# Kernel tuning notes

Hardware: AMD Instinct MI355X
Metric: run time of the kernel (lower is better)

## Reference

```python
import jax, jax.numpy as jnp
import numpy as np

NUM_HEADS = 12
HEAD_SIZE = 64  # hidden 768 / 12 heads


def setup_inputs() -> dict:
    key = jax.random.key(0)
    ks = jax.random.split(key, 5)
    B, M, P, H = 8, 4, 512, 768
    scale = 1.0 / np.sqrt(H)
    return {
        "hidden_states": jax.random.normal(ks[0], (B, M, P, H), dtype=jnp.float32),
        "Wq": jax.random.normal(ks[1], (H, H), dtype=jnp.float32) * scale,
        "bq": jnp.zeros((H,), dtype=jnp.float32),
        "Wk": jax.random.normal(ks[2], (H, H), dtype=jnp.float32) * scale,
        "bk": jnp.zeros((H,), dtype=jnp.float32),
        "Wv": jax.random.normal(ks[3], (H, H), dtype=jnp.float32) * scale,
        "bv": jnp.zeros((H,), dtype=jnp.float32),
        "Wo": jax.random.normal(ks[4], (H, H), dtype=jnp.float32) * scale,
        "bo": jnp.zeros((H,), dtype=jnp.float32),
    }


def reference(hidden_states, Wq, bq, Wk, bk, Wv, bv, Wo, bo):
    # hidden_states: [B, M, P, H] (batch, modalities, patches, hidden)
    B, M, P, H = hidden_states.shape
    nh, hs = NUM_HEADS, HEAD_SIZE

    def split_heads(x):  # [B,M,P,H] -> [B,M,nh,P,hs]
        return x.reshape(B, M, P, nh, hs).transpose(0, 1, 3, 2, 4)

    q = split_heads(hidden_states @ Wq + bq)
    k = split_heads(hidden_states @ Wk + bk)
    v = split_heads(hidden_states @ Wv + bv)

    # per-modality, per-head attention over patches
    scores = jnp.einsum('bmnqh,bmnkh->bmnqk', q, k) / np.sqrt(hs).astype(jnp.float32)
    probs = jax.nn.softmax(scores, axis=-1)  # [B,M,nh,P,P]
    ctx = jnp.einsum('bmnqk,bmnkh->bmnqh', probs, v)
    ctx = ctx.transpose(0, 1, 3, 2, 4).reshape(B, M, P, H)  # merge heads

    # output projection (dropout rate 0.0 -> identity)
    return ctx @ Wo + bo
```

## Files before the change

### kernel.cpp

```cpp
#include <hip/hip_runtime.h>
#include <cstdint>
#include <cstddef>

#define H_DIM 768
#define NHEADS 12
#define HSZ 64
#define PATCH 512
#define MTOT 16384
#define SZT ((long)MTOT * H_DIM)

using short8 = __attribute__((ext_vector_type(8))) short;
using f32x4  = __attribute__((ext_vector_type(4))) float;
using us4    = __attribute__((ext_vector_type(4))) unsigned short;

#define GLL16(gp, lp) __builtin_amdgcn_global_load_lds( \
    (const __attribute__((address_space(1))) void*)(gp), \
    (__attribute__((address_space(3))) void*)(lp), 16, 0, 0)

#define SB0() __builtin_amdgcn_sched_barrier(0)

__device__ __forceinline__ unsigned short bf16rne(float x) {
    unsigned v = __float_as_uint(x);
    v += 0x7fff + ((v >> 16) & 1);
    return (unsigned short)(v >> 16);
}

__global__ __launch_bounds__(256) void prep_all(
    const float* __restrict__ X, unsigned short* __restrict__ Xb,
    const float* __restrict__ Wq, const float* __restrict__ Wk,
    const float* __restrict__ Wv, const float* __restrict__ Wo,
    unsigned short* __restrict__ WqH, unsigned short* __restrict__ WkH,
    unsigned short* __restrict__ WvH, unsigned short* __restrict__ WoH)
{
    __shared__ float T[64][65];
    const int b = blockIdx.x;
    const int tid = threadIdx.x;

    if (b < 6144) {
        const long i = ((long)b * 256 + tid) * 8;
        float4 a = *(const float4*)&X[i];
        float4 c = *(const float4*)&X[i + 4];
        float xs[8] = {a.x, a.y, a.z, a.w, c.x, c.y, c.z, c.w};
        us4 h0, h1;
        #pragma unroll
        for (int j = 0; j < 4; ++j) { h0[j] = bf16rne(xs[j]); h1[j] = bf16rne(xs[j + 4]); }
        *(us4*)&Xb[i] = h0; *(us4*)&Xb[i + 4] = h1;
        return;
    }

    const int w     = b - 6144;
    const int which = w / 144;
    const int t     = w % 144;
    const int kt    = (t / 12) * 64, nt = (t % 12) * 64;
    const float* W  = (which == 0) ? Wq : (which == 1) ? Wk : (which == 2) ? Wv : Wo;
    unsigned short* Whi = (which == 0) ? WqH : (which == 1) ? WkH : (which == 2) ? WvH : WoH;

    const int r = tid >> 2, c16 = (tid & 3) * 16;
    #pragma unroll
    for (int j = 0; j < 4; ++j) {
        float4 v = *(const float4*)&W[(long)(kt + r) * H_DIM + nt + c16 + j * 4];
        T[r][c16 + j*4 + 0] = v.x; T[r][c16 + j*4 + 1] = v.y;
        T[r][c16 + j*4 + 2] = v.z; T[r][c16 + j*4 + 3] = v.w;
    }
    __syncthreads();
    unsigned short* ph = &Whi[(long)(nt + r) * H_DIM + kt + c16];
    #pragma unroll
    for (int j = 0; j < 16; ++j)
        ph[j] = bf16rne(T[c16 + j][r]);
}

__global__ __launch_bounds__(256, 2) void qkv_gemm(
    const unsigned short* __restrict__ Xb,
    const unsigned short* __restrict__ WqH, const unsigned short* __restrict__ WkH,
    const unsigned short* __restrict__ WvH,
    const float* __restrict__ bq, const float* __restrict__ bk, const float* __restrict__ bv,
    float qscale,
    unsigned short* __restrict__ Qt, unsigned short* __restrict__ Kp,
    unsigned short* __restrict__ Vp)
{
    __shared__ unsigned short As[16384];
    __shared__ unsigned short Bs[8192];

    const int s   = blockIdx.x;
    const int lid = (s & 7) * 144 + (s >> 3);
    const int bx  = lid % 18;
    const int by  = lid / 18;

    const int mat = bx / 6;
    const int n0  = (bx % 6) * 128;
    const int m0  = by * 256;
    const unsigned short* Bh = (mat == 0) ? WqH : (mat == 1) ? WkH : WvH;
    const float* bias        = (mat == 0) ? bq  : (mat == 1) ? bk  : bv;
    const float scale        = (mat == 0) ? qscale : 1.0f;

    const int tid  = threadIdx.x;
    const int lane = tid & 63;
    const int wv   = tid >> 6;
    const int wr   = wv >> 1, wc = wv & 1;
    const int q    = lane >> 4, l15 = lane & 15;

    const int srow   = tid >> 3;
    const int schunk = (tid & 7) ^ (srow & 7);

    char* ldsA = (char*)(&As[0]) + (wv << 10);
    char* ldsB = (char*)(&Bs[0]) + (wv << 10);

    f32x4 acc[8][4];
    #pragma unroll
    for (int i = 0; i < 8; ++i)
        #pragma unroll
        for (int j = 0; j < 4; ++j) acc[i][j] = 0;

    const int swz = (l15 & 7);

    for (int k0 = 0; k0 < H_DIM; k0 += 64) {
        #pragma unroll
        for (int i = 0; i < 8; ++i)
            GLL16(Xb + (long)(m0 + i * 32 + srow) * H_DIM + k0 + schunk * 8,
                  ldsA + i * 4096);
        #pragma unroll
        for (int i = 0; i < 4; ++i)
            GLL16(Bh + (long)(n0 + i * 32 + srow) * H_DIM + k0 + schunk * 8,
                  ldsB + i * 4096);
        __syncthreads();

        #pragma unroll
        for (int ks = 0; ks < 2; ++ks) {
            const int pc = ((ks * 4 + q) ^ swz) * 8;
            short8 ah[8], bh[4];
            #pragma unroll
            for (int t = 0; t < 8; ++t) {
                const int mr = wr * 128 + t * 16 + l15;
                ah[t] = *(const short8*)&As[mr * 64 + pc];
            }
            #pragma unroll
            for (int t = 0; t < 4; ++t) {
                const int nr = wc * 64 + t * 16 + l15;
                bh[t] = *(const short8*)&Bs[nr * 64 + pc];
            }
            #pragma unroll
            for (int mt = 0; mt < 8; ++mt)
                #pragma unroll
                for (int nt = 0; nt < 4; ++nt)
                    acc[mt][nt] = __builtin_amdgcn_mfma_f32_16x16x32_bf16(ah[mt], bh[nt], acc[mt][nt], 0, 0, 0);
        }
        __syncthreads();
    }

    #pragma unroll
    for (int nt = 0; nt < 4; ++nt) {
        const int col = n0 + wc * 64 + nt * 16 + l15;
        const float bcol = bias[col];
        const int h = col >> 6, d = col & 63;
        #pragma unroll
        for (int mt = 0; mt < 8; ++mt) {
            const int rowB = m0 + wr * 128 + mt * 16 + q * 4;
            #pragma unroll
            for (int r = 0; r < 4; ++r) {
                const int row = rowB + r;
                const float val = (acc[mt][nt][r] + bcol) * scale;
                const int bm = row >> 9, p = row & 511;
                const int bmh = bm * NHEADS + h;
                if (mat == 0) {
                    const long idx = ((long)bmh * 8 + (p >> 6)) * 4096 + (long)(p & 63) * 64 + d;
                    Qt[idx] = bf16rne(val);
                } else if (mat == 1) {
                    Kp[(long)bmh * 32768 + (long)p * 64 + d] = bf16rne(val);
                } else {
                    Vp[(long)bmh * 32768 + (long)d * 512 + p] = bf16rne(val);
                }
            }
        }
    }
}

__global__ __launch_bounds__(256, 3) void attn2(
    const unsigned short* __restrict__ Qt,
    const unsigned short* __restrict__ Kp, const unsigned short* __restrict__ Vp,
    unsigned short* __restrict__ Ctx)
{
    __shared__ unsigned short Ks[2][4096];
    __shared__ unsigned short Vs[2][4096];
    __shared__ unsigned short Ps[128 * 72];
    __shared__ float red[128][2];

    const int tid  = threadIdx.x;
    const int lane = tid & 63;
    const int wv   = tid >> 6;
    const int wr   = wv >> 1, wc = wv & 1;
    const int q    = lane >> 4, l15 = lane & 15;

    const int s   = blockIdx.x + 4 * blockIdx.y;
    const int lid = (s & 7) * 192 + (s >> 3);
    const int qt2 = lid & 3;
    const int bmh = lid >> 2;

    short8 qh[4][2];
    const long qtile = ((long)bmh * 8 + qt2 * 2 + wr) * 4096;
    #pragma unroll
    for (int mt = 0; mt < 4; ++mt)
        #pragma unroll
        for (int ks = 0; ks < 2; ++ks)
            qh[mt][ks] = *(const short8*)&Qt[qtile + (mt * 16 + l15) * 64 + ks * 32 + q * 8];

    f32x4 ctx[4][2];
    float l_cur[4][4];
    #pragma unroll
    for (int mt = 0; mt < 4; ++mt) {
        ctx[mt][0] = 0; ctx[mt][1] = 0;
        #pragma unroll
        for (int r = 0; r < 4; ++r) l_cur[mt][r] = 0.0f;
    }

    const long khead = (long)bmh * 32768;
    const int srow   = tid >> 3;
    const int gchunk = ((tid & 7) ^ (srow & 7)) * 8;
    char* dK = (char*)&Ks[0][0] + (wv << 10);
    char* dV = (char*)&Vs[0][0] + (wv << 10);

    #define STAGE_KV(kt_, bsel) do { \
        const long kb_ = khead + (long)(kt_) * 64 * 64; \
        GLL16(Kp + kb_ + (long)srow * 64 + gchunk,        dK + (bsel) * 8192); \
        GLL16(Kp + kb_ + (long)(srow + 32) * 64 + gchunk, dK + (bsel) * 8192 + 4096); \
        const long vb_ = khead + (long)(kt_) * 64; \
        GLL16(Vp + vb_ + (long)srow * 512 + gchunk,        dV + (bsel) * 8192); \
        GLL16(Vp + vb_ + (long)(srow + 32) * 512 + gchunk, dV + (bsel) * 8192 + 4096); \
    } while (0)

    STAGE_KV(0, 0);

    #pragma unroll 1
    for (int kt = 0; kt < 8; ++kt) {
        const int cur = kt & 1;
        asm volatile("s_waitcnt lgkmcnt(0)" ::: "memory");
        SB0();
        __builtin_amdgcn_s_barrier();
        if (kt < 7) {
            STAGE_KV(kt + 1, cur ^ 1);
            asm volatile("s_waitcnt vmcnt(4)" ::: "memory");
        } else {
            asm volatile("s_waitcnt vmcnt(0)" ::: "memory");
        }
        SB0();
        __builtin_amdgcn_s_barrier();

        f32x4 sv[4][2];
        #pragma unroll
        for (int mt = 0; mt < 4; ++mt) { sv[mt][0] = 0; sv[mt][1] = 0; }
        short8 kf[2][2];
        #pragma unroll
        for (int nt = 0; nt < 2; ++nt)
            #pragma unroll
            for (int ks = 0; ks < 2; ++ks) {
                const int key = wc * 32 + nt * 16 + l15;
                const int phys = (q + ks * 4) ^ (key & 7);
                kf[nt][ks] = *(const short8*)&Ks[cur][key * 64 + phys * 8];
            }
        #pragma unroll
        for (int mt = 0; mt < 4; ++mt)
            #pragma unroll
            for (int nt = 0; nt < 2; ++nt)
                #pragma unroll
                for (int ks = 0; ks < 2; ++ks)
                    sv[mt][nt] = __builtin_amdgcn_mfma_f32_16x16x32_bf16(qh[mt][ks], kf[nt][ks], sv[mt][nt], 0, 0, 0);

        #pragma unroll
        for (int mt = 0; mt < 4; ++mt)
            #pragma unroll
            for (int r = 0; r < 4; ++r) {
                const int row = wr * 64 + mt * 16 + q * 4 + r;
                const float p0 = __builtin_amdgcn_exp2f(sv[mt][0][r]);
                const float p1 = __builtin_amdgcn_exp2f(sv[mt][1][r]);
                l_cur[mt][r] += p0 + p1;
                Ps[row * 72 + wc * 32 + l15]      = bf16rne(p0);
                Ps[row * 72 + wc * 32 + 16 + l15] = bf16rne(p1);
            }
        asm volatile("s_waitcnt lgkmcnt(0)" ::: "memory");
        SB0();
        __builtin_amdgcn_s_barrier();

        short8 pf[4][2], vf[2][2];
        #pragma unroll
        for (int mt = 0; mt < 4; ++mt)
            #pragma unroll
            for (int ks = 0; ks < 2; ++ks)
                pf[mt][ks] = *(const short8*)&Ps[(wr * 64 + mt * 16 + l15) * 72 + ks * 32 + q * 8];
        #pragma unroll
        for (int nt = 0; nt < 2; ++nt)
            #pragma unroll
            for (int ks = 0; ks < 2; ++ks) {
                const int d = wc * 32 + nt * 16 + l15;
                const int phys = (q + ks * 4) ^ (d & 7);
                vf[nt][ks] = *(const short8*)&Vs[cur][d * 64 + phys * 8];
            }
        #pragma unroll
        for (int mt = 0; mt < 4; ++mt)
            #pragma unroll
            for (int nt = 0; nt < 2; ++nt)
                #pragma unroll
                for (int ks = 0; ks < 2; ++ks)
                    ctx[mt][nt] = __builtin_amdgcn_mfma_f32_16x16x32_bf16(pf[mt][ks], vf[nt][ks], ctx[mt][nt], 0, 0, 0);
    }
    #undef STAGE_KV

    #pragma unroll
    for (int mt = 0; mt < 4; ++mt)
        #pragma unroll
        for (int r = 0; r < 4; ++r) {
            float v = l_cur[mt][r];
            v += __shfl_xor(v, 1);
            v += __shfl_xor(v, 2);
            v += __shfl_xor(v, 4);
            v += __shfl_xor(v, 8);
            if (l15 == 0) red[wr * 64 + mt * 16 + q * 4 + r][wc] = v;
        }
    __syncthreads();
    #pragma unroll
    for (int mt = 0; mt < 4; ++mt)
        #pragma unroll
        for (int r = 0; r < 4; ++r) {
            const int row = wr * 64 + mt * 16 + q * 4 + r;
            const float2 rd = *(const float2*)&red[row][0];
            const float inv = 1.0f / (rd.x + rd.y);
            const int trow = mt * 16 + q * 4 + r;
            #pragma unroll
            for (int nt = 0; nt < 2; ++nt) {
                const int col = wc * 32 + nt * 16 + l15;
                Ctx[qtile + trow * 64 + col] = bf16rne(ctx[mt][nt][r] * inv);
            }
        }
}

__global__ __launch_bounds__(256, 4) void oproj(
    const unsigned short* __restrict__ Ctx,
    const unsigned short* __restrict__ WoH,
    const float* __restrict__ bo, float* __restrict__ out)
{
    __shared__ unsigned short As[8192];
    __shared__ unsigned short Bs[8192];

    const int tid  = threadIdx.x;
    const int lane = tid & 63;
    const int wv   = tid >> 6;
    const int wr   = wv >> 1, wc = wv & 1;
    const int q    = lane >> 4, l15 = lane & 15;

    const int s   = blockIdx.x + 6 * blockIdx.y;
    const int lid = (s & 7) * 96 + (s >> 3);
    const int n0  = (lid % 6) * 128;
    const int m0  = (lid / 6) * 128;

    const int srow   = tid >> 3;
    const int schunk = (tid & 7) ^ (srow & 7);

    char* ldsA = (char*)(&As[0]) + (wv << 10);
    char* ldsB = (char*)(&Bs[0]) + (wv << 10);

    f32x4 acc[4][4];
    #pragma unroll
    for (int i = 0; i < 4; ++i)
        #pragma unroll
        for (int j = 0; j < 4; ++j) acc[i][j] = 0;

    const int swz = (l15 & 7);

    for (int k0 = 0; k0 < H_DIM; k0 += 64) {
        const int h = k0 >> 6;
        #pragma unroll
        for (int i = 0; i < 4; ++i) {
            const int tok = m0 + i * 32 + srow;
            const long tile = ((long)(tok >> 9) * NHEADS + h) * 8 + ((tok >> 6) & 7);
            GLL16(Ctx + tile * 4096 + (long)(tok & 63) * 64 + schunk * 8, ldsA + i * 4096);
            GLL16(WoH + (long)(n0 + i * 32 + srow) * H_DIM + k0 + schunk * 8, ldsB + i * 4096);
        }
        __syncthreads();

        #pragma unroll
        for (int ks = 0; ks < 2; ++ks) {
            const int pc = ((ks * 4 + q) ^ swz) * 8;
            short8 ah[4], bh[4];
            #pragma unroll
            for (int t = 0; t < 4; ++t) {
                const int mr = wr * 64 + t * 16 + l15;
                ah[t] = *(const short8*)&As[mr * 64 + pc];
                const int nr = wc * 64 + t * 16 + l15;
                bh[t] = *(const short8*)&Bs[nr * 64 + pc];
            }
            #pragma unroll
            for (int mt = 0; mt < 4; ++mt)
                #pragma unroll
                for (int nt = 0; nt < 4; ++nt)
                    acc[mt][nt] = __builtin_amdgcn_mfma_f32_16x16x32_bf16(ah[mt], bh[nt], acc[mt][nt], 0, 0, 0);
        }
        __syncthreads();
    }

    #pragma unroll
    for (int nt = 0; nt < 4; ++nt) {
        const int col = n0 + wc * 64 + nt * 16 + l15;
        const float bcol = bo[col];
        #pragma unroll
        for (int mt = 0; mt < 4; ++mt) {
            const int rowB = m0 + wr * 64 + mt * 16 + q * 4;
            #pragma unroll
            for (int r = 0; r < 4; ++r)
                out[(long)(rowB + r) * H_DIM + col] = acc[mt][nt][r] + bcol;
        }
    }
}

extern "C" void kernel_launch(void* const* d_in, const int* in_sizes, int n_in,
                              void* d_out, int out_size, void* d_ws, size_t ws_size,
                              hipStream_t stream) {
    const float* X  = (const float*)d_in[0];
    const float* Wq = (const float*)d_in[1]; const float* bq = (const float*)d_in[2];
    const float* Wk = (const float*)d_in[3]; const float* bk = (const float*)d_in[4];
    const float* Wv = (const float*)d_in[5]; const float* bv = (const float*)d_in[6];
    const float* Wo = (const float*)d_in[7]; const float* bo = (const float*)d_in[8];

    unsigned short* wsu = (unsigned short*)d_ws;
    unsigned short* Qt  = wsu;
    unsigned short* Kp  = Qt + 12582912L;
    unsigned short* Vp  = Kp + 12582912L;
    unsigned short* Wt  = Vp + 12582912L;
    const long WP = (long)H_DIM * H_DIM;
    unsigned short* WqH = Wt;
    unsigned short* WkH = Wt + WP;
    unsigned short* WvH = Wt + 2 * WP;
    unsigned short* WoH = Wt + 3 * WP;

    unsigned short* Xb = (unsigned short*)d_out;

    prep_all<<<6720, 256, 0, stream>>>(X, Xb, Wq, Wk, Wv, Wo,
                                       WqH, WkH, WvH, WoH);

    const float qscale = 0.125f * 1.4426950408889634f;
    qkv_gemm<<<dim3(1152), 256, 0, stream>>>(Xb, WqH, WkH, WvH,
                                             bq, bk, bv, qscale, Qt, Kp, Vp);

    attn2<<<dim3(4, 384), 256, 0, stream>>>(Qt, Kp, Vp, Qt);

    oproj<<<dim3(6, 128), 256, 0, stream>>>(Qt, WoH, bo, (float*)d_out);
}
```

Measured before the change: 280.6 us.

## Drop K/V double buffering in attention to raise occupancy to four blocks

Attention K/V staging goes from two LDS buffers to one. Each key tile is now loaded synchronously between two block barriers instead of prefetching the next tile, and launch bounds rise from 3 to 4 blocks per CU. The goal is to shrink LDS per block so more blocks fit per CU and hide latency through occupancy rather than software pipelining. The cost is that global-to-LDS load latency is no longer overlapped within a block, and each iteration pays an extra full barrier.

```diff
diff --git a/kernel.cpp b/kernel.cpp
--- a/kernel.cpp
+++ b/kernel.cpp
@@ -174,13 +174,13 @@
     }
 }
 
-__global__ __launch_bounds__(256, 3) void attn2(
+__global__ __launch_bounds__(256, 4) void attn2(
     const unsigned short* __restrict__ Qt,
     const unsigned short* __restrict__ Kp, const unsigned short* __restrict__ Vp,
     unsigned short* __restrict__ Ctx)
 {
-    __shared__ unsigned short Ks[2][4096];
-    __shared__ unsigned short Vs[2][4096];
+    __shared__ unsigned short Ks[4096];
+    __shared__ unsigned short Vs[4096];
     __shared__ unsigned short Ps[128 * 72];
     __shared__ float red[128][2];
 
@@ -215,34 +215,20 @@
     const long khead = (long)bmh * 32768;
     const int srow   = tid >> 3;
     const int gchunk = ((tid & 7) ^ (srow & 7)) * 8;
-    char* dK = (char*)&Ks[0][0] + (wv << 10);
-    char* dV = (char*)&Vs[0][0] + (wv << 10);
-
-    #define STAGE_KV(kt_, bsel) do { \
-        const long kb_ = khead + (long)(kt_) * 64 * 64; \
-        GLL16(Kp + kb_ + (long)srow * 64 + gchunk,        dK + (bsel) * 8192); \
-        GLL16(Kp + kb_ + (long)(srow + 32) * 64 + gchunk, dK + (bsel) * 8192 + 4096); \
-        const long vb_ = khead + (long)(kt_) * 64; \
-        GLL16(Vp + vb_ + (long)srow * 512 + gchunk,        dV + (bsel) * 8192); \
-        GLL16(Vp + vb_ + (long)(srow + 32) * 512 + gchunk, dV + (bsel) * 8192 + 4096); \
-    } while (0)
-
-    STAGE_KV(0, 0);
-
-    #pragma unroll 1
+    char* dK = (char*)&Ks[0] + (wv << 10);
+    char* dV = (char*)&Vs[0] + (wv << 10);
+
     for (int kt = 0; kt < 8; ++kt) {
-        const int cur = kt & 1;
-        asm volatile("s_waitcnt lgkmcnt(0)" ::: "memory");
-        SB0();
-        __builtin_amdgcn_s_barrier();
-        if (kt < 7) {
-            STAGE_KV(kt + 1, cur ^ 1);
-            asm volatile("s_waitcnt vmcnt(4)" ::: "memory");
-        } else {
-            asm volatile("s_waitcnt vmcnt(0)" ::: "memory");
-        }
-        SB0();
-        __builtin_amdgcn_s_barrier();
+        __syncthreads();
+        {
+            const long kb = khead + (long)kt * 64 * 64;
+            GLL16(Kp + kb + (long)srow * 64 + gchunk,        dK);
+            GLL16(Kp + kb + (long)(srow + 32) * 64 + gchunk, dK + 4096);
+            const long vb = khead + (long)kt * 64;
+            GLL16(Vp + vb + (long)srow * 512 + gchunk,        dV);
+            GLL16(Vp + vb + (long)(srow + 32) * 512 + gchunk, dV + 4096);
+        }
+        __syncthreads();
 
         f32x4 sv[4][2];
         #pragma unroll
@@ -254,7 +240,7 @@
             for (int ks = 0; ks < 2; ++ks) {
                 const int key = wc * 32 + nt * 16 + l15;
                 const int phys = (q + ks * 4) ^ (key & 7);
-                kf[nt][ks] = *(const short8*)&Ks[cur][key * 64 + phys * 8];
+                kf[nt][ks] = *(const short8*)&Ks[key * 64 + phys * 8];
             }
         #pragma unroll
         for (int mt = 0; mt < 4; ++mt)
@@ -275,9 +261,7 @@
                 Ps[row * 72 + wc * 32 + l15]      = bf16rne(p0);
                 Ps[row * 72 + wc * 32 + 16 + l15] = bf16rne(p1);
             }
-        asm volatile("s_waitcnt lgkmcnt(0)" ::: "memory");
-        SB0();
-        __builtin_amdgcn_s_barrier();
+        __syncthreads();
 
         short8 pf[4][2], vf[2][2];
         #pragma unroll
@@ -291,7 +275,7 @@
             for (int ks = 0; ks < 2; ++ks) {
                 const int d = wc * 32 + nt * 16 + l15;
                 const int phys = (q + ks * 4) ^ (d & 7);
-                vf[nt][ks] = *(const short8*)&Vs[cur][d * 64 + phys * 8];
+                vf[nt][ks] = *(const short8*)&Vs[d * 64 + phys * 8];
             }
         #pragma unroll
         for (int mt = 0; mt < 4; ++mt)
@@ -301,7 +285,6 @@
                 for (int ks = 0; ks < 2; ++ks)
                     ctx[mt][nt] = __builtin_amdgcn_mfma_f32_16x16x32_bf16(pf[mt][ks], vf[nt][ks], ctx[mt][nt], 0, 0, 0);
     }
-    #undef STAGE_KV
 
     #pragma unroll
     for (int mt = 0; mt < 4; ++mt)
```

Measured after the change: 296.7 us. 1.06x slower.
